# Performance work log

Hardware: AMD Instinct MI355X
Metric: run time of the kernel (lower is better)

Reference implementation:

```python
import jax, jax.numpy as jnp
import numpy as np

HIDDEN = 896
N_HEADS = 14
N_KV_HEADS = 2
HEAD_DIM = HIDDEN // N_HEADS  # 64
ROPE_THETA = 1000000.0
B, S = 2, 2048


def setup_inputs() -> dict:
    key = jax.random.key(0)
    ks = jax.random.split(key, 8)
    hidden_states = jax.random.normal(ks[0], (B, S, HIDDEN), dtype=jnp.float32)
    # causal additive mask (1,1,S,S): 0 allowed, -1e9 masked
    causal = jnp.tril(jnp.ones((S, S), dtype=bool))
    attention_mask = jnp.where(causal, 0.0, -1e9).astype(jnp.float32)[None, None]
    sc = 1.0 / np.sqrt(HIDDEN)
    Wq = jax.random.normal(ks[1], (N_HEADS * HEAD_DIM, HIDDEN), dtype=jnp.float32) * sc
    bq = jnp.zeros((N_HEADS * HEAD_DIM,), dtype=jnp.float32)
    Wk = jax.random.normal(ks[2], (N_KV_HEADS * HEAD_DIM, HIDDEN), dtype=jnp.float32) * sc
    bk = jnp.zeros((N_KV_HEADS * HEAD_DIM,), dtype=jnp.float32)
    Wv = jax.random.normal(ks[3], (N_KV_HEADS * HEAD_DIM, HIDDEN), dtype=jnp.float32) * sc
    bv = jnp.zeros((N_KV_HEADS * HEAD_DIM,), dtype=jnp.float32)
    Wo = jax.random.normal(ks[4], (HIDDEN, N_HEADS * HEAD_DIM), dtype=jnp.float32) * sc
    return {"hidden_states": hidden_states, "attention_mask": attention_mask,
            "Wq": Wq, "bq": bq, "Wk": Wk, "bk": bk, "Wv": Wv, "bv": bv, "Wo": Wo}


def _rotate_half(x):
    h = x.shape[-1] // 2
    return jnp.concatenate((-x[..., h:], x[..., :h]), axis=-1)


def _rope_cos_sin(seq_len, dtype):
    inv_freq = 1.0 / (ROPE_THETA ** (jnp.arange(0, HEAD_DIM, 2, dtype=jnp.float32) / HEAD_DIM))
    t = jnp.arange(seq_len, dtype=jnp.float32)
    freqs = jnp.outer(t, inv_freq)                 # [S, D/2]
    emb = jnp.concatenate((freqs, freqs), axis=-1)  # [S, D]
    return jnp.cos(emb).astype(dtype)[None, None], jnp.sin(emb).astype(dtype)[None, None]


def reference(hidden_states, attention_mask, Wq, bq, Wk, bk, Wv, bv, Wo):
    b, s, _ = hidden_states.shape
    groups = N_HEADS // N_KV_HEADS
    q = (hidden_states @ Wq.T + bq).reshape(b, s, N_HEADS, HEAD_DIM).transpose(0, 2, 1, 3)
    k = (hidden_states @ Wk.T + bk).reshape(b, s, N_KV_HEADS, HEAD_DIM).transpose(0, 2, 1, 3)
    v = (hidden_states @ Wv.T + bv).reshape(b, s, N_KV_HEADS, HEAD_DIM).transpose(0, 2, 1, 3)
    cos, sin = _rope_cos_sin(s, q.dtype)
    q = q * cos + _rotate_half(q) * sin
    k = k * cos + _rotate_half(k) * sin
    k = jnp.repeat(k, groups, axis=1)  # GQA expand: [b, H, s, d]
    v = jnp.repeat(v, groups, axis=1)
    scores = jnp.einsum('bhqd,bhkd->bhqk', q, k) / np.sqrt(HEAD_DIM) + attention_mask
    w = jax.nn.softmax(scores.astype(jnp.float32), axis=-1).astype(q.dtype)
    out = jnp.einsum('bhqk,bhkd->bhqd', w, v)
    out = out.transpose(0, 2, 1, 3).reshape(b, s, HIDDEN)
    return out @ Wo.T
```

## Files before the change

kernel.cpp:

```cpp
#include <hip/hip_runtime.h>
#include <hip/hip_bf16.h>

#define BATCH 2
#define SEQ   2048
#define HID   896
#define NH    14
#define NKV   2
#define HDIM  64
#define GRP   7
#define ROWS  (BATCH*SEQ)
#define NQKV  1152

typedef float f32x4 __attribute__((ext_vector_type(4)));
typedef short s16x8 __attribute__((ext_vector_type(8)));
typedef unsigned short u16;

#define MFMA_BF16(a,b,c) __builtin_amdgcn_mfma_f32_16x16x32_bf16((a),(b),(c),0,0,0)

__device__ __forceinline__ u16 f2b(float f) {
  __hip_bfloat16 h = __float2bfloat16(f);
  return __builtin_bit_cast(u16, h);
}
__device__ __forceinline__ float b2f(u16 u) {
  unsigned v = ((unsigned)u) << 16;
  return __builtin_bit_cast(float, v);
}
__device__ __forceinline__ float fexp2(float x) {
  float r;
  asm("v_exp_f32 %0, %1" : "=v"(r) : "v"(x));
  return r;
}

__device__ __forceinline__ void gload16(const void* g, void* l) {
  __builtin_amdgcn_global_load_lds((const __attribute__((address_space(1))) void*)g,
                                   (__attribute__((address_space(3))) void*)l,
                                   16, 0, 0);
}

__device__ __forceinline__ int S8(int n) {
  if (n <= 8)  return n;
  if (n <= 16) return 2*n - 8;
  if (n <= 24) return 3*n - 24;
  return 4*n - 48;
}
__device__ __forceinline__ int prefJ(int qj) {
  const int n = qj >> 1;
  return 2*S8(n) + (qj & 1) * (1 + (n >> 3));
}

__global__ __launch_bounds__(256) void k_prep(const float* __restrict__ hidden,
                                              const float* __restrict__ Wq,
                                              const float* __restrict__ Wk,
                                              const float* __restrict__ Wv,
                                              const float* __restrict__ Wo,
                                              u16* __restrict__ hidB,
                                              u16* __restrict__ WqkvB,
                                              u16* __restrict__ WoB,
                                              float* __restrict__ ct,
                                              float* __restrict__ st) {
  const int bid = blockIdx.x, t = threadIdx.x;
  if (bid < 5376) {
    const float* src; u16* dst; int i;
    if (bid < 3584)      { src = hidden; dst = hidB;            i = bid*256 + t; }
    else if (bid < 4368) { src = Wq;     dst = WqkvB;           i = (bid-3584)*256 + t; }
    else if (bid < 4480) { src = Wk;     dst = WqkvB + 802816;  i = (bid-4368)*256 + t; }
    else if (bid < 4592) { src = Wv;     dst = WqkvB + 917504;  i = (bid-4480)*256 + t; }
    else                 { src = Wo;     dst = WoB;             i = (bid-4592)*256 + t; }
    float4 v = reinterpret_cast<const float4*>(src)[i];
    ushort4 o = { f2b(v.x), f2b(v.y), f2b(v.z), f2b(v.w) };
    reinterpret_cast<ushort4*>(dst)[i] = o;
  } else {
    const int i = (bid - 5376)*256 + t;
    const int s = i >> 5, fi = i & 31;
    double inv = exp(-(double)fi / 32.0 * log(1.0e6));
    double ang = (double)s * inv;
    ct[i] = (float)cos(ang);
    st[i] = (float)sin(ang);
  }
}

__global__ __launch_bounds__(256) void k_gemm_qkv(const u16* __restrict__ A,
                                                  const u16* __restrict__ Bt,
                                                  const float* __restrict__ bq,
                                                  const float* __restrict__ bk,
                                                  const float* __restrict__ bv,
                                                  const float* __restrict__ ct,
                                                  const float* __restrict__ st,
                                                  u16* __restrict__ Qr,
                                                  u16* __restrict__ Kf,
                                                  u16* __restrict__ Vf) {
  __shared__ __align__(16) u16 lA[2][128 * 32];
  __shared__ __align__(16) u16 lB[2][64 * 32];
  const int K = HID;
  const int t = threadIdx.x;
  const int l = t & 63, w = t >> 6;
  const int lr = l & 15, lg = l >> 4;
  const int bm = blockIdx.x * 128;
  const int hcol = blockIdx.y;
  const int srow = (l >> 2) & 3;
  const int sslot = (l & 3) ^ srow;
  const int rsw = (lr & 3);

  f32x4 acc[2][4] = {};

#define GSTAGE(buf, k0)                                                          \
  {                                                                              \
    _Pragma("unroll")                                                            \
    for (int i = 0; i < 2; ++i) {                                                \
      const int row = i*64 + w*16 + (l>>2);                                      \
      gload16(A + (size_t)(bm + row) * K + (k0) + sslot*8,                       \
              (char*)lA[buf] + i*4096 + w*1024);                                 \
    }                                                                            \
    gload16(Bt + (size_t)(hcol*64 + w*16 + (l>>2)) * K + (k0) + sslot*8,         \
            (char*)lB[buf] + w*1024);                                            \
  }

  int cur = 0;
  GSTAGE(0, 0);
  __syncthreads();
  for (int k0 = 0; k0 < K; k0 += 32) {
    if (k0 + 32 < K) GSTAGE(cur ^ 1, k0 + 32);
    const u16* lAc = lA[cur];
    const u16* lBc = lB[cur];
    s16x8 af[2], bf[4];
    #pragma unroll
    for (int m = 0; m < 2; ++m)
      af[m] = *(const s16x8*)&lAc[(w*32 + m*16 + lr)*32 + (lg ^ rsw)*8];
    #pragma unroll
    for (int n = 0; n < 4; ++n)
      bf[n] = *(const s16x8*)&lBc[(n*16 + lr)*32 + (lg ^ rsw)*8];
    #pragma unroll
    for (int m = 0; m < 2; ++m)
      #pragma unroll
      for (int n = 0; n < 4; ++n)
        acc[m][n] = MFMA_BF16(af[m], bf[n], acc[m][n]);
    __syncthreads();
    cur ^= 1;
  }
#undef GSTAGE

  const int bsel = bm >> 11;
  const float QSC = 0.125f * 1.44269504088896f;

  if (hcol < 14) {
    u16* qb = Qr + (size_t)(bsel*NH + hcol) * SEQ * HDIM;
    float bia0[2], bia2[2];
    #pragma unroll
    for (int n = 0; n < 2; ++n) {
      bia0[n] = bq[hcol*64 + n*16 + lr];
      bia2[n] = bq[hcol*64 + n*16 + lr + 32];
    }
    #pragma unroll
    for (int m = 0; m < 2; ++m)
      #pragma unroll
      for (int j = 0; j < 4; ++j) {
        const int s = (bm + w*32 + m*16 + lg*4 + j) & (SEQ - 1);
        #pragma unroll
        for (int n = 0; n < 2; ++n) {
          const int ic = n*16 + lr;
          const float c = ct[s*32 + ic], sv = st[s*32 + ic];
          const float x0 = acc[m][n][j] + bia0[n];
          const float x1 = acc[m][n+2][j] + bia2[n];
          qb[(size_t)s*HDIM + ic]      = f2b((x0*c - x1*sv) * QSC);
          qb[(size_t)s*HDIM + ic + 32] = f2b((x1*c + x0*sv) * QSC);
        }
      }
  } else if (hcol < 16) {
    const int hkk = hcol - 14;
    u16* kp = Kf + (size_t)(bsel*NKV + hkk) * SEQ * HDIM;
    float bia0[2], bia2[2];
    #pragma unroll
    for (int n = 0; n < 2; ++n) {
      bia0[n] = bk[hkk*64 + n*16 + lr];
      bia2[n] = bk[hkk*64 + n*16 + lr + 32];
    }
    #pragma unroll
    for (int m = 0; m < 2; ++m)
      #pragma unroll
      for (int j = 0; j < 4; ++j) {
        const int s = (bm + w*32 + m*16 + lg*4 + j) & (SEQ - 1);
        #pragma unroll
        for (int n = 0; n < 2; ++n) {
          const int d0 = n*16 + lr;
          const float c = ct[s*32 + d0], sv = st[s*32 + d0];
          const float x0 = acc[m][n][j] + bia0[n];
          const float x1 = acc[m][n+2][j] + bia2[n];
          const int off0 = (s>>4)*1024 + ((d0>>3)*128) + (s&15)*8 + (d0&7);
          kp[off0]       = f2b(x0*c - x1*sv);
          kp[off0 + 512] = f2b(x1*c + x0*sv);
        }
      }
  } else {
    const int hkk = hcol - 16;
    u16* vp = Vf + (size_t)(bsel*NKV + hkk) * SEQ * HDIM;
    float biav[4];
    #pragma unroll
    for (int n = 0; n < 4; ++n) biav[n] = bv[hkk*64 + n*16 + lr];
    #pragma unroll
    for (int m = 0; m < 2; ++m)
      #pragma unroll
      for (int j = 0; j < 4; ++j) {
        const int s = (bm + w*32 + m*16 + lg*4 + j) & (SEQ - 1);
        const int sbase = (s>>6)*4096 + ((s>>5)&1)*512 + ((s>>3)&3)*128 + (s&7);
        #pragma unroll
        for (int n = 0; n < 4; ++n)
          vp[sbase + n*1024 + lr*8] = f2b(acc[m][n][j] + biav[n]);
      }
  }
}

__global__ __launch_bounds__(256) void k_gemm_o(const u16* __restrict__ A,
                                                const u16* __restrict__ Bt,
                                                float* __restrict__ C,
                                                int N, int K) {
  __shared__ __align__(16) u16 lA[2][128 * 32];
  __shared__ __align__(16) u16 lB[2][64 * 32];
  const int t = threadIdx.x;
  const int l = t & 63, w = t >> 6;
  const int lr = l & 15, lg = l >> 4;
  const int bm = blockIdx.x * 128, bn = blockIdx.y * 64;
  const int srow = (l >> 2) & 3;
  const int sslot = (l & 3) ^ srow;
  const int rsw = (lr & 3);

  f32x4 acc[2][4] = {};

#define GSTAGE(buf, k0)                                                          \
  {                                                                              \
    _Pragma("unroll")                                                            \
    for (int i = 0; i < 2; ++i) {                                                \
      const int row = i*64 + w*16 + (l>>2);                                      \
      gload16(A + (size_t)(bm + row) * K + (k0) + sslot*8,                       \
              (char*)lA[buf] + i*4096 + w*1024);                                 \
    }                                                                            \
    gload16(Bt + (size_t)(bn + w*16 + (l>>2)) * K + (k0) + sslot*8,              \
            (char*)lB[buf] + w*1024);                                            \
  }

  int cur = 0;
  GSTAGE(0, 0);
  __syncthreads();
  for (int k0 = 0; k0 < K; k0 += 32) {
    if (k0 + 32 < K) GSTAGE(cur ^ 1, k0 + 32);
    const u16* lAc = lA[cur];
    const u16* lBc = lB[cur];
    s16x8 af[2], bf[4];
    #pragma unroll
    for (int m = 0; m < 2; ++m)
      af[m] = *(const s16x8*)&lAc[(w*32 + m*16 + lr)*32 + (lg ^ rsw)*8];
    #pragma unroll
    for (int n = 0; n < 4; ++n)
      bf[n] = *(const s16x8*)&lBc[(n*16 + lr)*32 + (lg ^ rsw)*8];
    #pragma unroll
    for (int m = 0; m < 2; ++m)
      #pragma unroll
      for (int n = 0; n < 4; ++n)
        acc[m][n] = MFMA_BF16(af[m], bf[n], acc[m][n]);
    __syncthreads();
    cur ^= 1;
  }
#undef GSTAGE

  #pragma unroll
  for (int n = 0; n < 4; ++n) {
    const int col = bn + n*16 + lr;
    #pragma unroll
    for (int m = 0; m < 2; ++m)
      #pragma unroll
      for (int j = 0; j < 4; ++j) {
        const int row = bm + w*32 + m*16 + lg*4 + j;
        C[(size_t)row * N + col] = acc[m][n][j];
      }
  }
}

__global__ __launch_bounds__(256, 3) void k_attn(const u16* __restrict__ Qr,
                                                 const u16* __restrict__ Kf,
                                                 const u16* __restrict__ Vf,
                                                 u16* __restrict__ pAcc,
                                                 float* __restrict__ pML) {
  __shared__ __align__(16) u16 lP[4][2048];

  const int t = threadIdx.x, l = t & 63, w = t >> 6;
  const int lr = l & 15, lg = l >> 4;
  const int g = blockIdx.x % 7;
  const int u = 159 - blockIdx.x / 7;
  int qj, ci;
  if (u < 16)       { qj = u;                 ci = 0; }
  else if (u < 48)  { qj = 16 + ((u-16)>>1);  ci = (u-16) & 1; }
  else if (u < 96)  { const int v = u - 48; const int q3 = v/3; qj = 32 + q3; ci = v - 3*q3; }
  else              { qj = 48 + ((u-96)>>2);  ci = (u-96) & 3; }

  const int bh = g*4 + w;
  const int b = bh / NH, h = bh % NH, hk = h / GRP;
  const int nt = (qj >> 1) + 1;
  const int kt0 = ci * 8;
  const int kt1 = min(nt, kt0 + 8);
  const int dt = nt - 1;
  const int qloc0 = (qj & 1) * 32;
  const int task = bh*160 + prefJ(qj) + ci;

  const u16* qb0 = Qr + ((size_t)((b*NH + h) * SEQ + qj*32 + lr)) * HDIM + lg*8;
  const s16x8 qf00 = *(const s16x8*)qb0;
  const s16x8 qf01 = *(const s16x8*)(qb0 + 32);
  const u16* qb1 = qb0 + 16 * HDIM;
  const s16x8 qf10 = *(const s16x8*)qb1;
  const s16x8 qf11 = *(const s16x8*)(qb1 + 32);

  const u16* kfp = Kf + (size_t)(b*NKV + hk) * SEQ * HDIM;
  const u16* vfp = Vf + (size_t)(b*NKV + hk) * SEQ * HDIM;

  f32x4 acc[8] = {};
  float lr0[4] = {0.f,0.f,0.f,0.f};
  float lr1[4] = {0.f,0.f,0.f,0.f};

  const int psw = (lr >> 2) << 4;

  for (int kt = kt0; kt < kt1; ++kt) {
    const u16* kbb = kfp + (size_t)kt*4096 + l*8;
    const s16x8 kf0 = *(const s16x8*)(kbb);
    const s16x8 kf1 = *(const s16x8*)(kbb + 512);
    const s16x8 kf2 = *(const s16x8*)(kbb + 1024);
    const s16x8 kf3 = *(const s16x8*)(kbb + 1536);
    const s16x8 kf4 = *(const s16x8*)(kbb + 2048);
    const s16x8 kf5 = *(const s16x8*)(kbb + 2560);
    const s16x8 kf6 = *(const s16x8*)(kbb + 3072);
    const s16x8 kf7 = *(const s16x8*)(kbb + 3584);

    f32x4 sc0[4], sc1[4];
    __builtin_amdgcn_s_setprio(1);
    {
      f32x4 a0={0.f,0.f,0.f,0.f}, a1={0.f,0.f,0.f,0.f}, a2={0.f,0.f,0.f,0.f}, a3={0.f,0.f,0.f,0.f};
      f32x4 b0={0.f,0.f,0.f,0.f}, b1={0.f,0.f,0.f,0.f}, b2={0.f,0.f,0.f,0.f}, b3={0.f,0.f,0.f,0.f};
      a0 = MFMA_BF16(qf00, kf0, a0); a0 = MFMA_BF16(qf01, kf1, a0);
      b0 = MFMA_BF16(qf10, kf0, b0); b0 = MFMA_BF16(qf11, kf1, b0);
      a1 = MFMA_BF16(qf00, kf2, a1); a1 = MFMA_BF16(qf01, kf3, a1);
      b1 = MFMA_BF16(qf10, kf2, b1); b1 = MFMA_BF16(qf11, kf3, b1);
      a2 = MFMA_BF16(qf00, kf4, a2); a2 = MFMA_BF16(qf01, kf5, a2);
      b2 = MFMA_BF16(qf10, kf4, b2); b2 = MFMA_BF16(qf11, kf5, b2);
      a3 = MFMA_BF16(qf00, kf6, a3); a3 = MFMA_BF16(qf01, kf7, a3);
      b3 = MFMA_BF16(qf10, kf6, b3); b3 = MFMA_BF16(qf11, kf7, b3);
      sc0[0]=a0; sc0[1]=a1; sc0[2]=a2; sc0[3]=a3;
      sc1[0]=b0; sc1[1]=b1; sc1[2]=b2; sc1[3]=b3;
    }
    __builtin_amdgcn_s_setprio(0);

    const u16* vbb = vfp + (size_t)kt*4096 + l*8;
    const s16x8 vv0 = *(const s16x8*)(vbb);
    const s16x8 vv1 = *(const s16x8*)(vbb + 512);
    const s16x8 vv2 = *(const s16x8*)(vbb + 1024);
    const s16x8 vv3 = *(const s16x8*)(vbb + 1536);
    const s16x8 vv4 = *(const s16x8*)(vbb + 2048);
    const s16x8 vv5 = *(const s16x8*)(vbb + 2560);
    const s16x8 vv6 = *(const s16x8*)(vbb + 3072);
    const s16x8 vv7 = *(const s16x8*)(vbb + 3584);

    if (kt == dt) {
      #pragma unroll
      for (int f = 0; f < 4; ++f)
        #pragma unroll
        for (int j = 0; j < 4; ++j) {
          if (f*16 + lr > qloc0      + lg*4 + j) sc0[f][j] = -1.0e9f;
          if (f*16 + lr > qloc0 + 16 + lg*4 + j) sc1[f][j] = -1.0e9f;
        }
    }

    u16* pw = lP[w];
    #pragma unroll
    for (int f = 0; f < 4; ++f)
      #pragma unroll
      for (int j = 0; j < 4; ++j) {
        const unsigned u0 = __builtin_bit_cast(unsigned, fexp2(sc0[f][j])) & 0xffff0000u;
        const unsigned u1 = __builtin_bit_cast(unsigned, fexp2(sc1[f][j])) & 0xffff0000u;
        lr0[j] += __builtin_bit_cast(float, u0);
        lr1[j] += __builtin_bit_cast(float, u1);
        const int ad = (lg*4 + j)*64 + ((f*16 + lr) ^ (lg << 4));
        pw[ad]        = (u16)(u0 >> 16);
        pw[1024 + ad] = (u16)(u1 >> 16);
      }
    const s16x8 pa00 = *(const s16x8*)&pw[lr*64 + ((lg*8     ) ^ psw)];
    const s16x8 pa01 = *(const s16x8*)&pw[lr*64 + ((32 + lg*8) ^ psw)];
    const s16x8 pa10 = *(const s16x8*)&pw[1024 + lr*64 + ((lg*8     ) ^ psw)];
    const s16x8 pa11 = *(const s16x8*)&pw[1024 + lr*64 + ((32 + lg*8) ^ psw)];

    __builtin_amdgcn_s_setprio(1);
    acc[0] = MFMA_BF16(pa00, vv0, acc[0]); acc[0] = MFMA_BF16(pa01, vv1, acc[0]);
    acc[4] = MFMA_BF16(pa10, vv0, acc[4]); acc[4] = MFMA_BF16(pa11, vv1, acc[4]);
    acc[1] = MFMA_BF16(pa00, vv2, acc[1]); acc[1] = MFMA_BF16(pa01, vv3, acc[1]);
    acc[5] = MFMA_BF16(pa10, vv2, acc[5]); acc[5] = MFMA_BF16(pa11, vv3, acc[5]);
    acc[2] = MFMA_BF16(pa00, vv4, acc[2]); acc[2] = MFMA_BF16(pa01, vv5, acc[2]);
    acc[6] = MFMA_BF16(pa10, vv4, acc[6]); acc[6] = MFMA_BF16(pa11, vv5, acc[6]);
    acc[3] = MFMA_BF16(pa00, vv6, acc[3]); acc[3] = MFMA_BF16(pa01, vv7, acc[3]);
    acc[7] = MFMA_BF16(pa10, vv6, acc[7]); acc[7] = MFMA_BF16(pa11, vv7, acc[7]);
    __builtin_amdgcn_s_setprio(0);
  }

  #pragma unroll
  for (int off = 1; off < 16; off <<= 1)
    #pragma unroll
    for (int j = 0; j < 4; ++j) {
      lr0[j] += __shfl_xor(lr0[j], off);
      lr1[j] += __shfl_xor(lr1[j], off);
    }

  u16* pa = pAcc + (size_t)task * 2048;
  #pragma unroll
  for (int df = 0; df < 4; ++df) {
    ushort4 o0 = { f2b(acc[df][0]), f2b(acc[df][1]), f2b(acc[df][2]), f2b(acc[df][3]) };
    ushort4 o1 = { f2b(acc[4+df][0]), f2b(acc[4+df][1]), f2b(acc[4+df][2]), f2b(acc[4+df][3]) };
    *reinterpret_cast<ushort4*>(pa + (df*64 + l)*4)        = o0;
    *reinterpret_cast<ushort4*>(pa + 1024 + (df*64 + l)*4) = o1;
  }
  if (lr == 0) {
    float* ml = pML + task * 32;
    #pragma unroll
    for (int j = 0; j < 4; ++j) {
      ml[lg*4 + j]      = lr0[j];
      ml[16 + lg*4 + j] = lr1[j];
    }
  }
}

__global__ __launch_bounds__(256) void k_reduce(const u16* __restrict__ pAcc,
                                                const float* __restrict__ pML,
                                                u16* __restrict__ Ao) {
  __shared__ __align__(16) u16 lT[4][2048];
  const int t = threadIdx.x, l = t & 63, w = t >> 6;
  const int lr = l & 15, lg = l >> 4;
  const int id = blockIdx.x * 4 + w;
  const int qj = id & 63, bh = id >> 6;
  const int b = bh / NH, h = bh % NH;
  const int nch = 1 + (qj >> 4);
  const int base = bh*160 + prefJ(qj);

  u16* lt = lT[w];
  #pragma unroll
  for (int frag = 0; frag < 2; ++frag) {
    float inv[4];
    #pragma unroll
    for (int j = 0; j < 4; ++j) {
      const int r = frag*16 + lg*4 + j;
      const float l0 = pML[(size_t)(base+0)*32 + r];
      const float l1 = (nch > 1) ? pML[(size_t)(base+1)*32 + r] : 0.f;
      const float l2 = (nch > 2) ? pML[(size_t)(base+2)*32 + r] : 0.f;
      const float l3 = (nch > 3) ? pML[(size_t)(base+3)*32 + r] : 0.f;
      inv[j] = 1.0f / (l0 + l1 + l2 + l3);
    }
    #pragma unroll
    for (int df = 0; df < 4; ++df) {
      const int eo = frag*1024 + (df*64 + l)*4;
      ushort4 a0 = *reinterpret_cast<const ushort4*>(pAcc + (size_t)(base+0)*2048 + eo);
      ushort4 a1 = (nch > 1) ? *reinterpret_cast<const ushort4*>(pAcc + (size_t)(base+1)*2048 + eo) : ushort4{0,0,0,0};
      ushort4 a2 = (nch > 2) ? *reinterpret_cast<const ushort4*>(pAcc + (size_t)(base+2)*2048 + eo) : ushort4{0,0,0,0};
      ushort4 a3 = (nch > 3) ? *reinterpret_cast<const ushort4*>(pAcc + (size_t)(base+3)*2048 + eo) : ushort4{0,0,0,0};
      const u16 e0[4] = {a0.x, a0.y, a0.z, a0.w};
      const u16 e1[4] = {a1.x, a1.y, a1.z, a1.w};
      const u16 e2[4] = {a2.x, a2.y, a2.z, a2.w};
      const u16 e3[4] = {a3.x, a3.y, a3.z, a3.w};
      #pragma unroll
      for (int j = 0; j < 4; ++j) {
        float o = (b2f(e0[j]) + b2f(e1[j]) + b2f(e2[j]) + b2f(e3[j])) * inv[j];
        lt[(frag*16 + lg*4 + j)*64 + df*16 + lr] = f2b(o);
      }
    }
  }

  const size_t orow = (size_t)b * SEQ + qj*32;
  #pragma unroll
  for (int i = 0; i < 4; ++i) {
    const int r = i*8 + (l >> 3);
    const s16x8 vrow = *(const s16x8*)&lt[r*64 + (l & 7)*8];
    *(s16x8*)&Ao[(orow + r) * HID + h*64 + (l & 7)*8] = vrow;
  }
}

extern "C" void kernel_launch(void* const* d_in, const int* in_sizes, int n_in,
                              void* d_out, int out_size, void* d_ws, size_t ws_size,
                              hipStream_t stream) {
  const float* hidden = (const float*)d_in[0];
  const float* Wq = (const float*)d_in[2];
  const float* bq = (const float*)d_in[3];
  const float* Wk = (const float*)d_in[4];
  const float* bk = (const float*)d_in[5];
  const float* Wv = (const float*)d_in[6];
  const float* bv = (const float*)d_in[7];
  const float* Wo = (const float*)d_in[8];

  char* ws = (char*)d_ws;
  u16*   hidB  = (u16*)(ws);
  u16*   Ao    = (u16*)(ws);
  u16*   WqkvB = (u16*)(ws + 7340032);
  u16*   WoB   = (u16*)(ws + 9404416);
  u16*   Qr    = (u16*)(ws + 11010048);
  u16*   Kf    = (u16*)(ws + 18350080);
  u16*   Vf    = (u16*)(ws + 19398656);
  float* ct    = (float*)(ws + 20447232);
  float* st    = (float*)(ws + 20709376);
  u16*   pAcc  = (u16*)(ws + 20971520);
  float* pML   = (float*)(ws + 39321600);

  k_prep<<<dim3(5632), dim3(256), 0, stream>>>(hidden, Wq, Wk, Wv, Wo,
                                               hidB, WqkvB, WoB, ct, st);
  k_gemm_qkv<<<dim3(32, 18), dim3(256), 0, stream>>>(hidB, WqkvB, bq, bk, bv,
                                                     ct, st, Qr, Kf, Vf);
  k_attn<<<dim3(1120), dim3(256), 0, stream>>>(Qr, Kf, Vf, pAcc, pML);
  k_reduce<<<dim3(448), dim3(256), 0, stream>>>(pAcc, pML, Ao);
  k_gemm_o<<<dim3(32, 14), dim3(256), 0, stream>>>(Ao, WoB, (float*)d_out, HID, HID);
}
```

Baseline: 90.94 us.

## Fuse hidden-state bf16 conversion into QKV GEMM and halve GEMM M-tiles

The separate fp32-to-bf16 pass over hidden_states in the prep kernel is removed. The QKV GEMM now loads fp32 activations directly into registers, converts them and stores them into LDS while computing the previous tile, which saves a full read and write of the activation buffer. Both GEMMs shrink their M tile from 128 to 64 rows, doubling the grid to fill more CUs. The cost is lower per-block arithmetic reuse and register-staged rather than async loads for the A operand.

```diff
diff --git a/kernel.cpp b/kernel.cpp
--- a/kernel.cpp
+++ b/kernel.cpp
@@ -37,6 +37,12 @@
                                    16, 0, 0);
 }
 
+__device__ __forceinline__ void pack8(const float4 x, const float4 y, u16* dst) {
+  u16 tmp[8] = { f2b(x.x), f2b(x.y), f2b(x.z), f2b(x.w),
+                 f2b(y.x), f2b(y.y), f2b(y.z), f2b(y.w) };
+  *(s16x8*)dst = *(const s16x8*)tmp;
+}
+
 __device__ __forceinline__ int S8(int n) {
   if (n <= 8)  return n;
   if (n <= 16) return 2*n - 8;
@@ -48,29 +54,26 @@
   return 2*S8(n) + (qj & 1) * (1 + (n >> 3));
 }
 
-__global__ __launch_bounds__(256) void k_prep(const float* __restrict__ hidden,
-                                              const float* __restrict__ Wq,
+__global__ __launch_bounds__(256) void k_prep(const float* __restrict__ Wq,
                                               const float* __restrict__ Wk,
                                               const float* __restrict__ Wv,
                                               const float* __restrict__ Wo,
-                                              u16* __restrict__ hidB,
                                               u16* __restrict__ WqkvB,
                                               u16* __restrict__ WoB,
                                               float* __restrict__ ct,
                                               float* __restrict__ st) {
   const int bid = blockIdx.x, t = threadIdx.x;
-  if (bid < 5376) {
+  if (bid < 1792) {
     const float* src; u16* dst; int i;
-    if (bid < 3584)      { src = hidden; dst = hidB;            i = bid*256 + t; }
-    else if (bid < 4368) { src = Wq;     dst = WqkvB;           i = (bid-3584)*256 + t; }
-    else if (bid < 4480) { src = Wk;     dst = WqkvB + 802816;  i = (bid-4368)*256 + t; }
-    else if (bid < 4592) { src = Wv;     dst = WqkvB + 917504;  i = (bid-4480)*256 + t; }
-    else                 { src = Wo;     dst = WoB;             i = (bid-4592)*256 + t; }
+    if (bid < 784)       { src = Wq; dst = WqkvB;           i = bid*256 + t; }
+    else if (bid < 896)  { src = Wk; dst = WqkvB + 802816;  i = (bid-784)*256 + t; }
+    else if (bid < 1008) { src = Wv; dst = WqkvB + 917504;  i = (bid-896)*256 + t; }
+    else                 { src = Wo; dst = WoB;             i = (bid-1008)*256 + t; }
     float4 v = reinterpret_cast<const float4*>(src)[i];
     ushort4 o = { f2b(v.x), f2b(v.y), f2b(v.z), f2b(v.w) };
     reinterpret_cast<ushort4*>(dst)[i] = o;
   } else {
-    const int i = (bid - 5376)*256 + t;
+    const int i = (bid - 1792)*256 + t;
     const int s = i >> 5, fi = i & 31;
     double inv = exp(-(double)fi / 32.0 * log(1.0e6));
     double ang = (double)s * inv;
@@ -79,7 +82,7 @@
   }
 }
 
-__global__ __launch_bounds__(256) void k_gemm_qkv(const u16* __restrict__ A,
+__global__ __launch_bounds__(256) void k_gemm_qkv(const float* __restrict__ A,
                                                   const u16* __restrict__ Bt,
                                                   const float* __restrict__ bq,
                                                   const float* __restrict__ bk,
@@ -89,55 +92,53 @@
                                                   u16* __restrict__ Qr,
                                                   u16* __restrict__ Kf,
                                                   u16* __restrict__ Vf) {
-  __shared__ __align__(16) u16 lA[2][128 * 32];
+  __shared__ __align__(16) u16 lA[2][64 * 32];
   __shared__ __align__(16) u16 lB[2][64 * 32];
-  const int K = HID;
   const int t = threadIdx.x;
   const int l = t & 63, w = t >> 6;
   const int lr = l & 15, lg = l >> 4;
-  const int bm = blockIdx.x * 128;
+  const int bm = blockIdx.x * 64;
   const int hcol = blockIdx.y;
-  const int srow = (l >> 2) & 3;
-  const int sslot = (l & 3) ^ srow;
+  const int srow = t >> 2;
+  const int ssl8 = ((t & 3) ^ (srow & 3)) * 8;
   const int rsw = (lr & 3);
 
-  f32x4 acc[2][4] = {};
-
-#define GSTAGE(buf, k0)                                                          \
-  {                                                                              \
-    _Pragma("unroll")                                                            \
-    for (int i = 0; i < 2; ++i) {                                                \
-      const int row = i*64 + w*16 + (l>>2);                                      \
-      gload16(A + (size_t)(bm + row) * K + (k0) + sslot*8,                       \
-              (char*)lA[buf] + i*4096 + w*1024);                                 \
-    }                                                                            \
-    gload16(Bt + (size_t)(hcol*64 + w*16 + (l>>2)) * K + (k0) + sslot*8,         \
-            (char*)lB[buf] + w*1024);                                            \
-  }
+  const float* ap = A + (size_t)(bm + srow) * HID + ssl8;
+  const u16*  bp = Bt + (size_t)(hcol*64 + srow) * HID + ssl8;
+  u16* lwA0 = &lA[0][srow*32 + (t & 3)*8];
+  u16* lwA1 = &lA[1][srow*32 + (t & 3)*8];
+
+  f32x4 acc[4] = {};
+
+  {
+    float4 a0 = *(const float4*)(ap);
+    float4 a1 = *(const float4*)(ap + 4);
+    gload16(bp, (char*)lB[0] + w*1024);
+    pack8(a0, a1, lwA0);
+  }
+  __syncthreads();
 
   int cur = 0;
-  GSTAGE(0, 0);
-  __syncthreads();
-  for (int k0 = 0; k0 < K; k0 += 32) {
-    if (k0 + 32 < K) GSTAGE(cur ^ 1, k0 + 32);
-    const u16* lAc = lA[cur];
-    const u16* lBc = lB[cur];
-    s16x8 af[2], bf[4];
-    #pragma unroll
-    for (int m = 0; m < 2; ++m)
-      af[m] = *(const s16x8*)&lAc[(w*32 + m*16 + lr)*32 + (lg ^ rsw)*8];
+  for (int k0 = 0; k0 < HID; k0 += 32) {
+    const bool nxt = (k0 + 32) < HID;
+    float4 a0, a1;
+    if (nxt) {
+      a0 = *(const float4*)(ap + k0 + 32);
+      a1 = *(const float4*)(ap + k0 + 36);
+      gload16(bp + k0 + 32, (char*)lB[cur ^ 1] + w*1024);
+    }
+    const s16x8 af = *(const s16x8*)&lA[cur][(w*16 + lr)*32 + (lg ^ rsw)*8];
+    s16x8 bf[4];
     #pragma unroll
     for (int n = 0; n < 4; ++n)
-      bf[n] = *(const s16x8*)&lBc[(n*16 + lr)*32 + (lg ^ rsw)*8];
-    #pragma unroll
-    for (int m = 0; m < 2; ++m)
-      #pragma unroll
-      for (int n = 0; n < 4; ++n)
-        acc[m][n] = MFMA_BF16(af[m], bf[n], acc[m][n]);
+      bf[n] = *(const s16x8*)&lB[cur][(n*16 + lr)*32 + (lg ^ rsw)*8];
+    #pragma unroll
+    for (int n = 0; n < 4; ++n)
+      acc[n] = MFMA_BF16(af, bf[n], acc[n]);
+    if (nxt) pack8(a0, a1, cur ? lwA0 : lwA1);
     __syncthreads();
     cur ^= 1;
   }
-#undef GSTAGE
 
   const int bsel = bm >> 11;
   const float QSC = 0.125f * 1.44269504088896f;
@@ -151,20 +152,18 @@
       bia2[n] = bq[hcol*64 + n*16 + lr + 32];
     }
     #pragma unroll
-    for (int m = 0; m < 2; ++m)
-      #pragma unroll
-      for (int j = 0; j < 4; ++j) {
-        const int s = (bm + w*32 + m*16 + lg*4 + j) & (SEQ - 1);
-        #pragma unroll
-        for (int n = 0; n < 2; ++n) {
-          const int ic = n*16 + lr;
-          const float c = ct[s*32 + ic], sv = st[s*32 + ic];
-          const float x0 = acc[m][n][j] + bia0[n];
-          const float x1 = acc[m][n+2][j] + bia2[n];
-          qb[(size_t)s*HDIM + ic]      = f2b((x0*c - x1*sv) * QSC);
-          qb[(size_t)s*HDIM + ic + 32] = f2b((x1*c + x0*sv) * QSC);
-        }
+    for (int j = 0; j < 4; ++j) {
+      const int s = (bm + w*16 + lg*4 + j) & (SEQ - 1);
+      #pragma unroll
+      for (int n = 0; n < 2; ++n) {
+        const int ic = n*16 + lr;
+        const float c = ct[s*32 + ic], sv = st[s*32 + ic];
+        const float x0 = acc[n][j] + bia0[n];
+        const float x1 = acc[n+2][j] + bia2[n];
+        qb[(size_t)s*HDIM + ic]      = f2b((x0*c - x1*sv) * QSC);
+        qb[(size_t)s*HDIM + ic + 32] = f2b((x1*c + x0*sv) * QSC);
       }
+    }
   } else if (hcol < 16) {
     const int hkk = hcol - 14;
     u16* kp = Kf + (size_t)(bsel*NKV + hkk) * SEQ * HDIM;
@@ -175,21 +174,19 @@
       bia2[n] = bk[hkk*64 + n*16 + lr + 32];
     }
     #pragma unroll
-    for (int m = 0; m < 2; ++m)
-      #pragma unroll
-      for (int j = 0; j < 4; ++j) {
-        const int s = (bm + w*32 + m*16 + lg*4 + j) & (SEQ - 1);
-        #pragma unroll
-        for (int n = 0; n < 2; ++n) {
-          const int d0 = n*16 + lr;
-          const float c = ct[s*32 + d0], sv = st[s*32 + d0];
-          const float x0 = acc[m][n][j] + bia0[n];
-          const float x1 = acc[m][n+2][j] + bia2[n];
-          const int off0 = (s>>4)*1024 + ((d0>>3)*128) + (s&15)*8 + (d0&7);
-          kp[off0]       = f2b(x0*c - x1*sv);
-          kp[off0 + 512] = f2b(x1*c + x0*sv);
-        }
+    for (int j = 0; j < 4; ++j) {
+      const int s = (bm + w*16 + lg*4 + j) & (SEQ - 1);
+      #pragma unroll
+      for (int n = 0; n < 2; ++n) {
+        const int d0 = n*16 + lr;
+        const float c = ct[s*32 + d0], sv = st[s*32 + d0];
+        const float x0 = acc[n][j] + bia0[n];
+        const float x1 = acc[n+2][j] + bia2[n];
+        const int off0 = (s>>4)*1024 + ((d0>>3)*128) + (s&15)*8 + (d0&7);
+        kp[off0]       = f2b(x0*c - x1*sv);
+        kp[off0 + 512] = f2b(x1*c + x0*sv);
       }
+    }
   } else {
     const int hkk = hcol - 16;
     u16* vp = Vf + (size_t)(bsel*NKV + hkk) * SEQ * HDIM;
@@ -197,15 +194,13 @@
     #pragma unroll
     for (int n = 0; n < 4; ++n) biav[n] = bv[hkk*64 + n*16 + lr];
     #pragma unroll
-    for (int m = 0; m < 2; ++m)
-      #pragma unroll
-      for (int j = 0; j < 4; ++j) {
-        const int s = (bm + w*32 + m*16 + lg*4 + j) & (SEQ - 1);
-        const int sbase = (s>>6)*4096 + ((s>>5)&1)*512 + ((s>>3)&3)*128 + (s&7);
-        #pragma unroll
-        for (int n = 0; n < 4; ++n)
-          vp[sbase + n*1024 + lr*8] = f2b(acc[m][n][j] + biav[n]);
-      }
+    for (int j = 0; j < 4; ++j) {
+      const int s = (bm + w*16 + lg*4 + j) & (SEQ - 1);
+      const int sbase = (s>>6)*4096 + ((s>>5)&1)*512 + ((s>>3)&3)*128 + (s&7);
+      #pragma unroll
+      for (int n = 0; n < 4; ++n)
+        vp[sbase + n*1024 + lr*8] = f2b(acc[n][j] + biav[n]);
+    }
   }
 }
 
@@ -213,64 +208,50 @@
                                                 const u16* __restrict__ Bt,
                                                 float* __restrict__ C,
                                                 int N, int K) {
-  __shared__ __align__(16) u16 lA[2][128 * 32];
+  __shared__ __align__(16) u16 lA[2][64 * 32];
   __shared__ __align__(16) u16 lB[2][64 * 32];
   const int t = threadIdx.x;
   const int l = t & 63, w = t >> 6;
   const int lr = l & 15, lg = l >> 4;
-  const int bm = blockIdx.x * 128, bn = blockIdx.y * 64;
-  const int srow = (l >> 2) & 3;
-  const int sslot = (l & 3) ^ srow;
+  const int bm = blockIdx.x * 64, bn = blockIdx.y * 64;
+  const int srow = t >> 2;
+  const int ssl8 = ((t & 3) ^ (srow & 3)) * 8;
   const int rsw = (lr & 3);
 
-  f32x4 acc[2][4] = {};
-
-#define GSTAGE(buf, k0)                                                          \
-  {                                                                              \
-    _Pragma("unroll")                                                            \
-    for (int i = 0; i < 2; ++i) {                                                \
-      const int row = i*64 + w*16 + (l>>2);                                      \
-      gload16(A + (size_t)(bm + row) * K + (k0) + sslot*8,                       \
-              (char*)lA[buf] + i*4096 + w*1024);                                 \
-    }                                                                            \
-    gload16(Bt + (size_t)(bn + w*16 + (l>>2)) * K + (k0) + sslot*8,              \
-            (char*)lB[buf] + w*1024);                                            \
-  }
-
+  const u16* apb = A + (size_t)(bm + srow) * K + ssl8;
+  const u16* bpb = Bt + (size_t)(bn + srow) * K + ssl8;
+
+  f32x4 acc[4] = {};
+
+  gload16(apb, (char*)lA[0] + w*1024);
+  gload16(bpb, (char*)lB[0] + w*1024);
+  __syncthreads();
   int cur = 0;
-  GSTAGE(0, 0);
-  __syncthreads();
   for (int k0 = 0; k0 < K; k0 += 32) {
-    if (k0 + 32 < K) GSTAGE(cur ^ 1, k0 + 32);
-    const u16* lAc = lA[cur];
-    const u16* lBc = lB[cur];
-    s16x8 af[2], bf[4];
-    #pragma unroll
-    for (int m = 0; m < 2; ++m)
-      af[m] = *(const s16x8*)&lAc[(w*32 + m*16 + lr)*32 + (lg ^ rsw)*8];
+    if (k0 + 32 < K) {
+      gload16(apb + k0 + 32, (char*)lA[cur ^ 1] + w*1024);
+      gload16(bpb + k0 + 32, (char*)lB[cur ^ 1] + w*1024);
+    }
+    const s16x8 af = *(const s16x8*)&lA[cur][(w*16 + lr)*32 + (lg ^ rsw)*8];
+    s16x8 bf[4];
     #pragma unroll
     for (int n = 0; n < 4; ++n)
-      bf[n] = *(const s16x8*)&lBc[(n*16 + lr)*32 + (lg ^ rsw)*8];
-    #pragma unroll
-    for (int m = 0; m < 2; ++m)
-      #pragma unroll
-      for (int n = 0; n < 4; ++n)
-        acc[m][n] = MFMA_BF16(af[m], bf[n], acc[m][n]);
+      bf[n] = *(const s16x8*)&lB[cur][(n*16 + lr)*32 + (lg ^ rsw)*8];
+    #pragma unroll
+    for (int n = 0; n < 4; ++n)
+      acc[n] = MFMA_BF16(af, bf[n], acc[n]);
     __syncthreads();
     cur ^= 1;
   }
-#undef GSTAGE
 
   #pragma unroll
   for (int n = 0; n < 4; ++n) {
     const int col = bn + n*16 + lr;
     #pragma unroll
-    for (int m = 0; m < 2; ++m)
-      #pragma unroll
-      for (int j = 0; j < 4; ++j) {
-        const int row = bm + w*32 + m*16 + lg*4 + j;
-        C[(size_t)row * N + col] = acc[m][n][j];
-      }
+    for (int j = 0; j < 4; ++j) {
+      const int row = bm + w*16 + lg*4 + j;
+      C[(size_t)row * N + col] = acc[n][j];
+    }
   }
 }
 
@@ -487,7 +468,6 @@
   const float* Wo = (const float*)d_in[8];
 
   char* ws = (char*)d_ws;
-  u16*   hidB  = (u16*)(ws);
   u16*   Ao    = (u16*)(ws);
   u16*   WqkvB = (u16*)(ws + 7340032);
   u16*   WoB   = (u16*)(ws + 9404416);
@@ -499,11 +479,11 @@
   u16*   pAcc  = (u16*)(ws + 20971520);
   float* pML   = (float*)(ws + 39321600);
 
-  k_prep<<<dim3(5632), dim3(256), 0, stream>>>(hidden, Wq, Wk, Wv, Wo,
-                                               hidB, WqkvB, WoB, ct, st);
-  k_gemm_qkv<<<dim3(32, 18), dim3(256), 0, stream>>>(hidB, WqkvB, bq, bk, bv,
+  k_prep<<<dim3(2048), dim3(256), 0, stream>>>(Wq, Wk, Wv, Wo,
+                                               WqkvB, WoB, ct, st);
+  k_gemm_qkv<<<dim3(64, 18), dim3(256), 0, stream>>>(hidden, WqkvB, bq, bk, bv,
                                                      ct, st, Qr, Kf, Vf);
   k_attn<<<dim3(1120), dim3(256), 0, stream>>>(Qr, Kf, Vf, pAcc, pML);
   k_reduce<<<dim3(448), dim3(256), 0, stream>>>(pAcc, pML, Ao);
-  k_gemm_o<<<dim3(32, 14), dim3(256), 0, stream>>>(Ao, WoB, (float*)d_out, HID, HID);
-}
+  k_gemm_o<<<dim3(64, 14), dim3(256), 0, stream>>>(Ao, WoB, (float*)d_out, HID, HID);
+}
```

Measured after the change: 92.14 us. No clear change (+1.3%).
